# Optimization experiments

Measured on AMD Instinct MI355X. Metric: run time of the kernel, lower is better.

## Reference

```python
import jax, jax.numpy as jnp
import numpy as np

N_NODES = 50000
N_EDGES = 600000
N_RELS = 16
N_GRAPHS = 128
IN_DIM = 128
REL_LAYERS = [128, 256, 128]
HIDDEN = [128, 256, 128]
N_CLASSES = 8


def setup_inputs() -> dict:
    key = jax.random.key(0)
    ks = jax.random.split(key, 24)
    inp = {}
    inp["h"] = jax.random.normal(ks[0], (N_NODES, IN_DIM), dtype=jnp.float32)
    inp["src"] = jax.random.randint(ks[1], (N_EDGES,), 0, N_NODES)
    inp["dst"] = jax.random.randint(ks[2], (N_EDGES,), 0, N_NODES)
    inp["rel_types"] = jax.random.randint(ks[3], (N_EDGES,), 0, N_RELS)
    inp["graph_ids"] = jnp.sort(jax.random.randint(ks[4], (N_NODES,), 0, N_GRAPHS))
    # RelGraphConv params per layer: W_rel [R,din,dout], W_loop [din,dout], b [dout]
    prev = IN_DIM
    ki = 5
    for i, d in enumerate(REL_LAYERS):
        inp[f"W_rel{i}"] = jax.random.normal(ks[ki], (N_RELS, prev, d), dtype=jnp.float32) * 0.05
        inp[f"W_loop{i}"] = jax.random.normal(ks[ki + 1], (prev, d), dtype=jnp.float32) * 0.05
        inp[f"b{i}"] = jnp.zeros((d,), dtype=jnp.float32)
        prev = d
        ki += 2
    for i, d in enumerate(HIDDEN):
        inp[f"Wh{i}"] = jax.random.normal(ks[ki], (prev, d), dtype=jnp.float32) * 0.05
        inp[f"bh{i}"] = jnp.zeros((d,), dtype=jnp.float32)
        prev = d
        ki += 1
    inp["Wc"] = jax.random.normal(ks[ki], (prev, N_CLASSES), dtype=jnp.float32) * 0.05
    inp["bc"] = jnp.zeros((N_CLASSES,), dtype=jnp.float32)
    return inp


def _rel_graph_conv(h, src, dst, rel, W_rel, W_loop, b):
    # transform every node under every relation: [R, N, dout]
    t = jnp.einsum("nd,rde->rne", h, W_rel)
    msgs = t[rel, src]  # [E, dout] gather per edge
    agg = jax.ops.segment_sum(msgs, dst, num_segments=h.shape[0])
    return jax.nn.relu(agg + h @ W_loop + b)  # self-loop + bias (DGL defaults)


def _forward(h, src, dst, rel_types, graph_ids,
             W_rel0, W_loop0, b0, W_rel1, W_loop1, b1, W_rel2, W_loop2, b2,
             Wh0, bh0, Wh1, bh1, Wh2, bh2, Wc, bc):
    h = h.astype(jnp.float32)
    for Wr, Wl, b in ((W_rel0, W_loop0, b0), (W_rel1, W_loop1, b1), (W_rel2, W_loop2, b2)):
        h = _rel_graph_conv(h, src, dst, rel_types, Wr, Wl, b)
    # dgl.mean_nodes: per-graph mean pooling
    sums = jax.ops.segment_sum(h, graph_ids, num_segments=N_GRAPHS)
    cnts = jax.ops.segment_sum(jnp.ones((h.shape[0],), h.dtype), graph_ids, num_segments=N_GRAPHS)
    hg = sums / jnp.maximum(cnts, 1.0)[:, None]
    for W, b in ((Wh0, bh0), (Wh1, bh1), (Wh2, bh2)):
        hg = jax.nn.relu(hg @ W + b)
    return jax.nn.softmax(hg @ Wc + bc, axis=1)


def reference(h, src, dst, rel_types, graph_ids,
              W_rel0, W_loop0, b0, W_rel1, W_loop1, b1, W_rel2, W_loop2, b2,
              Wh0, bh0, Wh1, bh1, Wh2, bh2, Wc, bc):
    return _forward(h, src, dst, rel_types, graph_ids,
                    W_rel0, W_loop0, b0, W_rel1, W_loop1, b1, W_rel2, W_loop2, b2,
                    Wh0, bh0, Wh1, bh1, Wh2, bh2, Wc, bc)
```

## Files before the change

### kernel.cpp

```cpp
#include <hip/hip_runtime.h>
#include <stdint.h>

#define NN 50000
#define NE 600000
#define NR 16
#define NG 128
#define TS 128
#define SCAN_B 512
#define NB_SCAN ((NN + SCAN_B - 1) / SCAN_B)
#define MAXB 1024

typedef short bf16x8 __attribute__((ext_vector_type(8)));
typedef float f32x4 __attribute__((ext_vector_type(4)));

static __device__ __forceinline__ unsigned short f2bf(float x) {
    unsigned int b = __float_as_uint(x);
    b += 0x7FFFu + ((b >> 16) & 1u);
    return (unsigned short)(b >> 16);
}
static __device__ __forceinline__ float bf2f(unsigned short u) {
    return __uint_as_float(((unsigned int)u) << 16);
}


__global__ void k_hist(const int* __restrict__ rel, const int* __restrict__ dst,
                       int* __restrict__ bcnt, int* __restrict__ ncnt, int npc, int B) {
    __shared__ int lh[MAXB];
    for (int i = threadIdx.x; i < B; i += 256) lh[i] = 0;
    __syncthreads();
    for (int e = blockIdx.x * blockDim.x + threadIdx.x; e < NE; e += gridDim.x * blockDim.x) {
        int d = dst[e];
        atomicAdd(&lh[(d / npc) * NR + rel[e]], 1);
        atomicAdd(&ncnt[d], 1);
    }
    __syncthreads();
    for (int i = threadIdx.x; i < B; i += 256) atomicAdd(&bcnt[i], lh[i]);
}

__global__ void k_scan1(const int* __restrict__ ncnt, int* __restrict__ bsum) {
    __shared__ int s[SCAN_B];
    int i = blockIdx.x * SCAN_B + threadIdx.x;
    s[threadIdx.x] = (i < NN) ? ncnt[i] : 0;
    __syncthreads();
    for (int off = SCAN_B / 2; off > 0; off >>= 1) {
        if (threadIdx.x < off) s[threadIdx.x] += s[threadIdx.x + off];
        __syncthreads();
    }
    if (threadIdx.x == 0) bsum[blockIdx.x] = s[0];
}

__global__ void k_scan2(const int* __restrict__ bsum, int* __restrict__ bpref, int* __restrict__ rowptr) {
    if (threadIdx.x == 0 && blockIdx.x == 0) {
        int run = 0;
        for (int b = 0; b < NB_SCAN; ++b) { bpref[b] = run; run += bsum[b]; }
        rowptr[NN] = run;
    }
}

__global__ void k_scan3(const int* __restrict__ ncnt, const int* __restrict__ bpref,
                        int* __restrict__ rowptr) {
    __shared__ int s[SCAN_B];
    int i = blockIdx.x * SCAN_B + threadIdx.x;
    int val = (i < NN) ? ncnt[i] : 0;
    s[threadIdx.x] = val;
    __syncthreads();
    for (int off = 1; off < SCAN_B; off <<= 1) {
        int x = (threadIdx.x >= off) ? s[threadIdx.x - off] : 0;
        __syncthreads();
        s[threadIdx.x] += x;
        __syncthreads();
    }
    if (i < NN) rowptr[i] = bpref[blockIdx.x] + s[threadIdx.x] - val;
}

__global__ __launch_bounds__(1024)
void k_scan_buckets(const int* __restrict__ bcnt, int B, int npc,
                    const int* __restrict__ rowptr,
                    int* __restrict__ boff, int* __restrict__ tstart,
                    int4* __restrict__ tilemap) {
    __shared__ int s1[MAXB], s2[MAXB];
    __shared__ int e_ex[MAXB + 1], t_ex[MAXB + 1];
    int tid = threadIdx.x;
    int v1 = (tid < B) ? bcnt[tid] : 0;
    int v2 = (v1 + TS - 1) / TS;
    s1[tid] = v1; s2[tid] = v2;
    __syncthreads();
    for (int off = 1; off < MAXB; off <<= 1) {
        int a1 = (tid >= off) ? s1[tid - off] : 0;
        int a2 = (tid >= off) ? s2[tid - off] : 0;
        __syncthreads();
        s1[tid] += a1; s2[tid] += a2;
        __syncthreads();
    }
    if (tid < B) {
        e_ex[tid] = s1[tid] - v1;
        t_ex[tid] = s2[tid] - v2;
        boff[tid] = e_ex[tid];
        tstart[tid] = t_ex[tid];
        if (tid == B - 1) {
            e_ex[B] = s1[tid]; t_ex[B] = s2[tid];
            boff[B] = s1[tid]; tstart[B] = s2[tid];
        }
    }
    __syncthreads();
    int T = t_ex[B];
    for (int t = tid; t < T; t += 1024) {
        int lo = 0, hi = B - 1;
        while (lo < hi) {
            int mid = (lo + hi + 1) >> 1;
            if (t_ex[mid] <= t) lo = mid; else hi = mid - 1;
        }
        int b = lo;
        int tt = t - t_ex[b];
        int v1b = e_ex[b + 1] - e_ex[b];
        int rem = v1b - tt * TS;
        int cnt = rem < TS ? rem : TS;
        int chunk = b >> 4;
        int nstart = chunk * npc; if (nstart > NN) nstart = NN;
        tilemap[t] = make_int4(b & (NR - 1), e_ex[b] + tt * TS, cnt, rowptr[nstart]);
    }
}

__global__ void k_scatter(const int* __restrict__ rel, const int* __restrict__ dst,
                          const int* __restrict__ src,
                          const int* __restrict__ boff, int* __restrict__ cursor,
                          const int* __restrict__ rowptr, int* __restrict__ ncur,
                          int* __restrict__ srcs, int* __restrict__ dpos, int npc, int B) {
    __shared__ int lh[MAXB];
    const int CH = 4096;
    int e0 = blockIdx.x * CH;
    for (int i = threadIdx.x; i < B; i += 256) lh[i] = 0;
    __syncthreads();
    for (int i = threadIdx.x; i < CH; i += 256) {
        int e = e0 + i;
        if (e < NE) atomicAdd(&lh[(dst[e] / npc) * NR + rel[e]], 1);
    }
    __syncthreads();
    for (int i = threadIdx.x; i < B; i += 256) {
        int c = lh[i];
        lh[i] = (c > 0) ? atomicAdd(&cursor[i], c) : 0;
    }
    __syncthreads();
    for (int i = threadIdx.x; i < CH; i += 256) {
        int e = e0 + i;
        if (e < NE) {
            int d = dst[e];
            int b = (d / npc) * NR + rel[e];
            int p = boff[b] + atomicAdd(&lh[b], 1);
            int pd = rowptr[d] + atomicAdd(&ncur[d], 1);
            srcs[p] = src[e];
            dpos[p] = pd;
        }
    }
}


__global__ void k_hconv(const float* __restrict__ h, unsigned short* __restrict__ hb, int n4) {
    int i = blockIdx.x * 256 + threadIdx.x;
    if (i < n4) {
        float4 v = reinterpret_cast<const float4*>(h)[i];
        ushort4 o = { f2bf(v.x), f2bf(v.y), f2bf(v.z), f2bf(v.w) };
        reinterpret_cast<ushort4*>(hb)[i] = o;
    }
}

__global__ void k_wconv_all(const float* Wr0, const float* Wr1, const float* Wr2,
                            const float* Wl0, const float* Wl1, const float* Wl2,
                            unsigned short* Wt0, unsigned short* Wt1, unsigned short* Wt2,
                            unsigned short* Wlt0, unsigned short* Wlt1, unsigned short* Wlt2) {
    const float* W; unsigned short* O; int R, Kd, Nd;
    switch (blockIdx.y) {
        case 0:  W = Wr0; O = Wt0;  R = NR; Kd = 128; Nd = 128; break;
        case 1:  W = Wr1; O = Wt1;  R = NR; Kd = 128; Nd = 256; break;
        case 2:  W = Wr2; O = Wt2;  R = NR; Kd = 256; Nd = 128; break;
        case 3:  W = Wl0; O = Wlt0; R = 1;  Kd = 128; Nd = 128; break;
        case 4:  W = Wl1; O = Wlt1; R = 1;  Kd = 128; Nd = 256; break;
        default: W = Wl2; O = Wlt2; R = 1;  Kd = 256; Nd = 128; break;
    }
    int total = R * Kd * Nd;
    for (int i = blockIdx.x * 256 + threadIdx.x; i < total; i += gridDim.x * 256) {
        int r = i / (Kd * Nd);
        int rem = i - r * Kd * Nd;
        int k = rem / Nd;
        int n = rem - k * Nd;
        O[((size_t)r * Nd + n) * Kd + k] = f2bf(W[i]);
    }
}


template<int K>
__global__ __launch_bounds__(256, 4)
void k_dense_mfma(const unsigned short* __restrict__ hb,
                  const unsigned short* __restrict__ Wlt,
                  const float* __restrict__ bias,
                  float* __restrict__ outbuf, int ldn) {
    __shared__ __align__(16) unsigned short As[128][72];
    __shared__ __align__(16) unsigned short Bs[128][72];
    const int tid = threadIdx.x;
    const int row0 = blockIdx.x * 128;
    const int colbase = blockIdx.y * 128;
    const int lane = tid & 63, w = tid >> 6;
    const int quad = lane >> 4, col = lane & 15;
    const int srow = tid >> 3, sk = (tid & 7) * 8;

    f32x4 acc[8][2];
#pragma unroll
    for (int i = 0; i < 8; ++i) { acc[i][0] = 0.f; acc[i][1] = 0.f; }

    for (int k0 = 0; k0 < K; k0 += 64) {
        __syncthreads();
#pragma unroll
        for (int pp = 0; pp < 4; ++pp) {
            int rw = pp * 32 + srow;
            int ar = row0 + rw; if (ar >= NN) ar = NN - 1;
            *reinterpret_cast<uint4*>(&As[rw][sk]) =
                *reinterpret_cast<const uint4*>(hb + (size_t)ar * K + k0 + sk);
            *reinterpret_cast<uint4*>(&Bs[rw][sk]) =
                *reinterpret_cast<const uint4*>(Wlt + (size_t)(colbase + rw) * K + k0 + sk);
        }
        __syncthreads();
#pragma unroll
        for (int s = 0; s < 2; ++s) {
            bf16x8 bf0 = *reinterpret_cast<const bf16x8*>(&Bs[w * 32 + col][s * 32 + quad * 8]);
            bf16x8 bf1 = *reinterpret_cast<const bf16x8*>(&Bs[w * 32 + 16 + col][s * 32 + quad * 8]);
#pragma unroll
            for (int rt = 0; rt < 8; ++rt) {
                bf16x8 af = *reinterpret_cast<const bf16x8*>(&As[rt * 16 + col][s * 32 + quad * 8]);
                acc[rt][0] = __builtin_amdgcn_mfma_f32_16x16x32_bf16(af, bf0, acc[rt][0], 0, 0, 0);
                acc[rt][1] = __builtin_amdgcn_mfma_f32_16x16x32_bf16(af, bf1, acc[rt][1], 0, 0, 0);
            }
        }
    }
    float bv0 = bias[colbase + w * 32 + col];
    float bv1 = bias[colbase + w * 32 + 16 + col];
#pragma unroll
    for (int rt = 0; rt < 8; ++rt) {
#pragma unroll
        for (int reg = 0; reg < 4; ++reg) {
            int r = row0 + rt * 16 + quad * 4 + reg;
            if (r < NN) {
                float* dp = outbuf + (size_t)r * ldn + colbase + w * 32;
                dp[col] = acc[rt][0][reg] + bv0;
                dp[16 + col] = acc[rt][1][reg] + bv1;
            }
        }
    }
}


template<int K>
__global__ __launch_bounds__(256, 4)
void k_edge_mfma(const unsigned short* __restrict__ hb,
                 const unsigned short* __restrict__ Wt,
                 int ldn, int colbase,
                 const int* __restrict__ srcs, const int* __restrict__ dpos,
                 const int4* __restrict__ tilemap, const int* __restrict__ tstart,
                 int chunkBase,
                 unsigned short* __restrict__ msg, int capRows) {
    const int tb0 = tstart[chunkBase];
    const int tend = tstart[chunkBase + NR];
    const int t = tb0 + blockIdx.x;
    if (t >= tend) return;
    const int4 tm = tilemap[t];
    const int r = tm.x, e0 = tm.y, cnt = tm.z, cES = tm.w;

    __shared__ __align__(16) unsigned short As[2][128][72];
    __shared__ int s_src[TS], s_out[TS];
    const int tid = threadIdx.x;
    if (tid < TS) {
        int ei = e0 + (tid < cnt ? tid : cnt - 1);
        s_src[tid] = srcs[ei];
        int row = dpos[ei] - cES;
        s_out[tid] = (tid < cnt && row < capRows) ? row : -1;
    }
    __syncthreads();

    const unsigned short* Wb = Wt + ((size_t)r * ldn + colbase) * K;
    const int lane = tid & 63, w = tid >> 6;
    const int quad = lane >> 4, col = lane & 15;
    const int srow = tid >> 3, sk = (tid & 7) * 8;

    int myrow[4];
#pragma unroll
    for (int q = 0; q < 4; ++q) myrow[q] = s_src[q * 32 + srow];

    f32x4 acc[8][2];
#pragma unroll
    for (int i = 0; i < 8; ++i) { acc[i][0] = 0.f; acc[i][1] = 0.f; }

    const int NCH = K / 64;
    {
        uint4 v[4];
#pragma unroll
        for (int q = 0; q < 4; ++q)
            v[q] = *reinterpret_cast<const uint4*>(hb + (size_t)myrow[q] * K + sk);
#pragma unroll
        for (int q = 0; q < 4; ++q)
            *reinterpret_cast<uint4*>(&As[0][q * 32 + srow][sk]) = v[q];
    }
    __syncthreads();
#pragma unroll
    for (int c = 0; c < NCH; ++c) {
        uint4 v[4];
        if (c + 1 < NCH) {
#pragma unroll
            for (int q = 0; q < 4; ++q)
                v[q] = *reinterpret_cast<const uint4*>(hb + (size_t)myrow[q] * K + (c + 1) * 64 + sk);
        }
#pragma unroll
        for (int k32 = 0; k32 < 2; ++k32) {
            bf16x8 bf0 = *reinterpret_cast<const bf16x8*>(
                Wb + (size_t)(w * 32 + col) * K + c * 64 + k32 * 32 + quad * 8);
            bf16x8 bf1 = *reinterpret_cast<const bf16x8*>(
                Wb + (size_t)(w * 32 + 16 + col) * K + c * 64 + k32 * 32 + quad * 8);
#pragma unroll
            for (int rt = 0; rt < 8; ++rt) {
                bf16x8 af = *reinterpret_cast<const bf16x8*>(&As[c & 1][rt * 16 + col][k32 * 32 + quad * 8]);
                acc[rt][0] = __builtin_amdgcn_mfma_f32_16x16x32_bf16(af, bf0, acc[rt][0], 0, 0, 0);
                acc[rt][1] = __builtin_amdgcn_mfma_f32_16x16x32_bf16(af, bf1, acc[rt][1], 0, 0, 0);
            }
        }
        if (c + 1 < NCH) {
#pragma unroll
            for (int q = 0; q < 4; ++q)
                *reinterpret_cast<uint4*>(&As[(c + 1) & 1][q * 32 + srow][sk]) = v[q];
        }
        __syncthreads();
    }
#pragma unroll
    for (int rt = 0; rt < 8; ++rt) {
#pragma unroll
        for (int reg = 0; reg < 4; ++reg) {
            int m = rt * 16 + quad * 4 + reg;
            int o = s_out[m];
            if (o >= 0) {
                unsigned short* dp = msg + (size_t)o * 128 + w * 32;
                dp[col] = f2bf(acc[rt][0][reg]);
                dp[16 + col] = f2bf(acc[rt][1][reg]);
            }
        }
    }
}

__global__ __launch_bounds__(256)
void k_reduce(const unsigned short* __restrict__ msg,
              const float* __restrict__ selfb, int ld_self, int co_self,
              unsigned short* __restrict__ out_bf, int ld_bf, int co_bf,
              float* __restrict__ out_f32, int ld_f32, int co_f32,
              const int* __restrict__ rowptr, int n0, int npc, int capRows) {
    int idx = blockIdx.x * 4 + (threadIdx.x >> 6);
    int n = n0 + idx;
    if (idx >= npc || n >= NN) return;
    int lane = threadIdx.x & 63;
    int cES = rowptr[n0];
    float2 acc = *reinterpret_cast<const float2*>(selfb + (size_t)n * ld_self + co_self + lane * 2);
    int j0 = rowptr[n], j1 = rowptr[n + 1];
    for (int j = j0; j < j1; ++j) {
        int rr = j - cES;
        if (rr >= capRows) break;
        unsigned int m = *reinterpret_cast<const unsigned int*>(msg + (size_t)rr * 128 + lane * 2);
        acc.x += bf2f((unsigned short)(m & 0xffffu));
        acc.y += bf2f((unsigned short)(m >> 16));
    }
    acc.x = acc.x > 0.f ? acc.x : 0.f;
    acc.y = acc.y > 0.f ? acc.y : 0.f;
    if (out_bf) {
        unsigned int o = (unsigned int)f2bf(acc.x) | ((unsigned int)f2bf(acc.y) << 16);
        *reinterpret_cast<unsigned int*>(out_bf + (size_t)n * ld_bf + co_bf + lane * 2) = o;
    }
    if (out_f32) {
        *reinterpret_cast<float2*>(out_f32 + (size_t)n * ld_f32 + co_f32 + lane * 2) = acc;
    }
}


__global__ void k_pool(const float* __restrict__ h, const int* __restrict__ gid,
                       float* __restrict__ hg, float* __restrict__ gcnt) {
    const int c = threadIdx.x;
    int n0 = blockIdx.x * 64;
    if (n0 >= NN) return;
    int end = n0 + 64; if (end > NN) end = NN;
    int cur = gid[n0];
    float run = 0.f, crun = 0.f;
    for (int n = n0; n < end; ++n) {
        int g = gid[n];
        if (g != cur) {
            atomicAdd(&hg[cur * 128 + c], run);
            if (c == 0) atomicAdd(&gcnt[cur], crun);
            run = 0.f; crun = 0.f; cur = g;
        }
        run += h[(size_t)n * 128 + c];
        crun += 1.f;
    }
    atomicAdd(&hg[cur * 128 + c], run);
    if (c == 0) atomicAdd(&gcnt[cur], crun);
}

__global__ __launch_bounds__(256)
void k_head(const float* __restrict__ hg, const float* __restrict__ gcnt,
            const float* __restrict__ Wh0, const float* __restrict__ bh0,
            const float* __restrict__ Wh1, const float* __restrict__ bh1,
            const float* __restrict__ Wh2, const float* __restrict__ bh2,
            const float* __restrict__ Wc, const float* __restrict__ bc,
            float* __restrict__ out) {
    __shared__ float x0[128], x1[128], x2[256], x3[128], sl[8];
    int g = blockIdx.x, t = threadIdx.x;
    if (t < 128) {
        float c = gcnt[g];
        x0[t] = hg[g * 128 + t] / (c > 1.f ? c : 1.f);
    }
    __syncthreads();
    if (t < 128) {
        float a = bh0[t];
        for (int k = 0; k < 128; ++k) a += x0[k] * Wh0[k * 128 + t];
        x1[t] = a > 0.f ? a : 0.f;
    }
    __syncthreads();
    {
        float a = bh1[t];
        for (int k = 0; k < 128; ++k) a += x1[k] * Wh1[k * 256 + t];
        x2[t] = a > 0.f ? a : 0.f;
    }
    __syncthreads();
    if (t < 128) {
        float a = bh2[t];
        for (int k = 0; k < 256; ++k) a += x2[k] * Wh2[k * 128 + t];
        x3[t] = a > 0.f ? a : 0.f;
    }
    __syncthreads();
    if (t < 8) {
        float a = bc[t];
        for (int k = 0; k < 128; ++k) a += x3[k] * Wc[k * 8 + t];
        sl[t] = a;
    }
    __syncthreads();
    if (t == 0) {
        float m = sl[0];
        for (int c = 1; c < 8; ++c) m = sl[c] > m ? sl[c] : m;
        float s = 0.f, e[8];
        for (int c = 0; c < 8; ++c) { e[c] = expf(sl[c] - m); s += e[c]; }
        for (int c = 0; c < 8; ++c) out[g * 8 + c] = e[c] / s;
    }
}


extern "C" void kernel_launch(void* const* d_in, const int* in_sizes, int n_in,
                              void* d_out, int out_size, void* d_ws, size_t ws_size,
                              hipStream_t stream) {
    const float* h0   = (const float*)d_in[0];
    const int* src    = (const int*)d_in[1];
    const int* dst    = (const int*)d_in[2];
    const int* rel    = (const int*)d_in[3];
    const int* gid    = (const int*)d_in[4];
    const float* Wr0  = (const float*)d_in[5];
    const float* Wl0  = (const float*)d_in[6];
    const float* b0   = (const float*)d_in[7];
    const float* Wr1  = (const float*)d_in[8];
    const float* Wl1  = (const float*)d_in[9];
    const float* b1   = (const float*)d_in[10];
    const float* Wr2  = (const float*)d_in[11];
    const float* Wl2  = (const float*)d_in[12];
    const float* b2   = (const float*)d_in[13];
    const float* Wh0  = (const float*)d_in[14];
    const float* bh0  = (const float*)d_in[15];
    const float* Wh1  = (const float*)d_in[16];
    const float* bh1  = (const float*)d_in[17];
    const float* Wh2  = (const float*)d_in[18];
    const float* bh2  = (const float*)d_in[19];
    const float* Wc   = (const float*)d_in[20];
    const float* bc   = (const float*)d_in[21];
    float* out = (float*)d_out;

    char* p = (char*)d_ws;
    auto alloc = [&](size_t bytes) { char* q = p; p += (bytes + 255) & ~(size_t)255; return q; };
    float* bufS  = (float*)alloc((size_t)NN * 256 * 4);
    unsigned short* hbA = (unsigned short*)alloc((size_t)NN * 256 * 2);
    unsigned short* hbB = (unsigned short*)alloc((size_t)NN * 128 * 2);
    unsigned short* Wt0 = (unsigned short*)alloc((size_t)NR * 128 * 128 * 2);
    unsigned short* Wt1 = (unsigned short*)alloc((size_t)NR * 256 * 128 * 2);
    unsigned short* Wt2 = (unsigned short*)alloc((size_t)NR * 128 * 256 * 2);
    unsigned short* Wlt0 = (unsigned short*)alloc((size_t)128 * 128 * 2);
    unsigned short* Wlt1 = (unsigned short*)alloc((size_t)256 * 128 * 2);
    unsigned short* Wlt2 = (unsigned short*)alloc((size_t)128 * 256 * 2);
    int* srcs    = (int*)alloc((size_t)NE * 4);
    int* dpos    = (int*)alloc((size_t)NE * 4);
    int* rowptr  = (int*)alloc((size_t)(NN + 1) * 4);
    int* bsum    = (int*)alloc(NB_SCAN * 4);
    int* bpref   = (int*)alloc(NB_SCAN * 4);
    int* boff    = (int*)alloc((MAXB + 1) * 4);
    int* tstart  = (int*)alloc((MAXB + 1) * 4);
    int4* tilemap = (int4*)alloc((size_t)(NE / TS + MAXB + 64) * 16);
    char* zbase  = p;
    int* bcnt    = (int*)alloc(MAXB * 4);
    int* cursor  = (int*)alloc(MAXB * 4);
    int* ncnt    = (int*)alloc((size_t)NN * 4);
    int* ncur    = (int*)alloc((size_t)NN * 4);
    float* hg    = (float*)alloc((size_t)NG * 128 * 4);
    float* gcnt  = (float*)alloc(NG * 4);
    size_t zlen  = (size_t)(p - zbase);
    unsigned short* msg = (unsigned short*)p;

    long long avail = (long long)ws_size - (long long)(p - (char*)d_ws);
    if (avail < (1 << 20)) avail = (1 << 20);
    long long capR64 = avail / 256;
    int C = 64;
    for (int c = 1; c <= 64; ++c) {
        double need = (double)NE / c * 1.15 + 4096.0;
        if ((double)capR64 >= need) { C = c; break; }
    }
    int npc = (NN + C - 1) / C;
    int B = C * NR;
    int capRows = capR64 > 2000000000LL ? 2000000000 : (int)capR64;
    int TPC = (int)((double)NE / C * 1.15 / TS) + NR + 8;
    int RDB = (npc + 3) / 4;

    hipMemsetAsync(zbase, 0, zlen, stream);
    k_hist<<<256, 256, 0, stream>>>(rel, dst, bcnt, ncnt, npc, B);
    k_scan1<<<NB_SCAN, SCAN_B, 0, stream>>>(ncnt, bsum);
    k_scan2<<<1, 64, 0, stream>>>(bsum, bpref, rowptr);
    k_scan3<<<NB_SCAN, SCAN_B, 0, stream>>>(ncnt, bpref, rowptr);
    k_scan_buckets<<<1, MAXB, 0, stream>>>(bcnt, B, npc, rowptr, boff, tstart, tilemap);
    k_scatter<<<(NE + 4095) / 4096, 256, 0, stream>>>(rel, dst, src, boff, cursor, rowptr, ncur, srcs, dpos, npc, B);

    k_hconv<<<(NN * 128 / 4 + 255) / 256, 256, 0, stream>>>(h0, hbA, NN * 128 / 4);
    k_wconv_all<<<dim3(512, 6), 256, 0, stream>>>(Wr0, Wr1, Wr2, Wl0, Wl1, Wl2,
                                                  Wt0, Wt1, Wt2, Wlt0, Wlt1, Wlt2);

    const int RB = (NN + TS - 1) / TS;

    k_dense_mfma<128><<<dim3(RB, 1), 256, 0, stream>>>(hbA, Wlt0, b0, bufS, 128);
    for (int c = 0; c < C; ++c) {
        k_edge_mfma<128><<<TPC, 256, 0, stream>>>(hbA, Wt0, 128, 0, srcs, dpos, tilemap, tstart, c * NR, msg, capRows);
        k_reduce<<<RDB, 256, 0, stream>>>(msg, bufS, 128, 0, hbB, 128, 0, (float*)nullptr, 0, 0, rowptr, c * npc, npc, capRows);
    }

    k_dense_mfma<128><<<dim3(RB, 2), 256, 0, stream>>>(hbB, Wlt1, b1, bufS, 256);
    for (int half = 0; half < 2; ++half) {
        for (int c = 0; c < C; ++c) {
            k_edge_mfma<128><<<TPC, 256, 0, stream>>>(hbB, Wt1, 256, half * 128, srcs, dpos, tilemap, tstart, c * NR, msg, capRows);
            k_reduce<<<RDB, 256, 0, stream>>>(msg, bufS, 256, half * 128, hbA, 256, half * 128, (float*)nullptr, 0, 0, rowptr, c * npc, npc, capRows);
        }
    }

    k_dense_mfma<256><<<dim3(RB, 1), 256, 0, stream>>>(hbA, Wlt2, b2, bufS, 128);
    for (int c = 0; c < C; ++c) {
        k_edge_mfma<256><<<TPC, 256, 0, stream>>>(hbA, Wt2, 128, 0, srcs, dpos, tilemap, tstart, c * NR, msg, capRows);
        k_reduce<<<RDB, 256, 0, stream>>>(msg, bufS, 128, 0, (unsigned short*)nullptr, 0, 0, bufS, 128, 0, rowptr, c * npc, npc, capRows);
    }

    k_pool<<<(NN + 63) / 64, 128, 0, stream>>>(bufS, gid, hg, gcnt);
    k_head<<<NG, 256, 0, stream>>>(hg, gcnt, Wh0, bh0, Wh1, bh1, Wh2, bh2, Wc, bc, out);
}
```

Measured before the change: 815.7 us.

## Process two edge tiles per block, single-buffer LDS, unroll reduce loop

The edge kernel now handles two tilemap tiles per block with a single LDS buffer and half the grid. The old double-buffered prefetch of the next K-chunk is replaced by a load-sync-compute sequence. The reduce kernel clamps the row bound once and unrolls the message accumulation by four so more loads are in flight. Fewer blocks and less LDS may help occupancy and launch cost, but dropping the prefetch exposes gather latency and halves block-level parallelism.

```diff
diff --git a/kernel.cpp b/kernel.cpp
--- a/kernel.cpp
+++ b/kernel.cpp
@@ -259,84 +259,75 @@
                  unsigned short* __restrict__ msg, int capRows) {
     const int tb0 = tstart[chunkBase];
     const int tend = tstart[chunkBase + NR];
-    const int t = tb0 + blockIdx.x;
-    if (t >= tend) return;
-    const int4 tm = tilemap[t];
-    const int r = tm.x, e0 = tm.y, cnt = tm.z, cES = tm.w;
-
-    __shared__ __align__(16) unsigned short As[2][128][72];
-    __shared__ int s_src[TS], s_out[TS];
+    const int t0 = tb0 + blockIdx.x * 2;
+    if (t0 >= tend) return;
+    const int nt = (t0 + 1 < tend) ? 2 : 1;
+
+    __shared__ __align__(16) unsigned short As[128][72];
+    __shared__ int4 s_tm[2];
+    __shared__ int s_src[2][TS], s_out[2][TS];
     const int tid = threadIdx.x;
-    if (tid < TS) {
-        int ei = e0 + (tid < cnt ? tid : cnt - 1);
-        s_src[tid] = srcs[ei];
-        int row = dpos[ei] - cES;
-        s_out[tid] = (tid < cnt && row < capRows) ? row : -1;
-    }
-    __syncthreads();
-
-    const unsigned short* Wb = Wt + ((size_t)r * ldn + colbase) * K;
+    {
+        int ti = tid >> 7;
+        int li = tid & 127;
+        if (ti < nt) {
+            int4 tm = tilemap[t0 + ti];
+            if (li == 0) s_tm[ti] = tm;
+            int ei = tm.y + (li < tm.z ? li : tm.z - 1);
+            s_src[ti][li] = srcs[ei];
+            int row = dpos[ei] - tm.w;
+            s_out[ti][li] = (li < tm.z && row < capRows) ? row : -1;
+        }
+    }
+    __syncthreads();
+
     const int lane = tid & 63, w = tid >> 6;
     const int quad = lane >> 4, col = lane & 15;
     const int srow = tid >> 3, sk = (tid & 7) * 8;
 
-    int myrow[4];
-#pragma unroll
-    for (int q = 0; q < 4; ++q) myrow[q] = s_src[q * 32 + srow];
-
-    f32x4 acc[8][2];
-#pragma unroll
-    for (int i = 0; i < 8; ++i) { acc[i][0] = 0.f; acc[i][1] = 0.f; }
-
-    const int NCH = K / 64;
-    {
-        uint4 v[4];
-#pragma unroll
-        for (int q = 0; q < 4; ++q)
-            v[q] = *reinterpret_cast<const uint4*>(hb + (size_t)myrow[q] * K + sk);
-#pragma unroll
-        for (int q = 0; q < 4; ++q)
-            *reinterpret_cast<uint4*>(&As[0][q * 32 + srow][sk]) = v[q];
-    }
-    __syncthreads();
-#pragma unroll
-    for (int c = 0; c < NCH; ++c) {
-        uint4 v[4];
-        if (c + 1 < NCH) {
+    for (int ti = 0; ti < nt; ++ti) {
+        const int r = s_tm[ti].x;
+        const unsigned short* Wb = Wt + ((size_t)r * ldn + colbase) * K;
+        int myrow[4];
+#pragma unroll
+        for (int q = 0; q < 4; ++q) myrow[q] = s_src[ti][q * 32 + srow];
+
+        f32x4 acc[8][2];
+#pragma unroll
+        for (int i = 0; i < 8; ++i) { acc[i][0] = 0.f; acc[i][1] = 0.f; }
+
+        for (int k0 = 0; k0 < K; k0 += 64) {
+            if (k0 + ti) __syncthreads();
 #pragma unroll
             for (int q = 0; q < 4; ++q)
-                v[q] = *reinterpret_cast<const uint4*>(hb + (size_t)myrow[q] * K + (c + 1) * 64 + sk);
-        }
-#pragma unroll
-        for (int k32 = 0; k32 < 2; ++k32) {
-            bf16x8 bf0 = *reinterpret_cast<const bf16x8*>(
-                Wb + (size_t)(w * 32 + col) * K + c * 64 + k32 * 32 + quad * 8);
-            bf16x8 bf1 = *reinterpret_cast<const bf16x8*>(
-                Wb + (size_t)(w * 32 + 16 + col) * K + c * 64 + k32 * 32 + quad * 8);
-#pragma unroll
-            for (int rt = 0; rt < 8; ++rt) {
-                bf16x8 af = *reinterpret_cast<const bf16x8*>(&As[c & 1][rt * 16 + col][k32 * 32 + quad * 8]);
-                acc[rt][0] = __builtin_amdgcn_mfma_f32_16x16x32_bf16(af, bf0, acc[rt][0], 0, 0, 0);
-                acc[rt][1] = __builtin_amdgcn_mfma_f32_16x16x32_bf16(af, bf1, acc[rt][1], 0, 0, 0);
+                *reinterpret_cast<uint4*>(&As[q * 32 + srow][sk]) =
+                    *reinterpret_cast<const uint4*>(hb + (size_t)myrow[q] * K + k0 + sk);
+            __syncthreads();
+#pragma unroll
+            for (int k32 = 0; k32 < 2; ++k32) {
+                bf16x8 bf0 = *reinterpret_cast<const bf16x8*>(
+                    Wb + (size_t)(w * 32 + col) * K + k0 + k32 * 32 + quad * 8);
+                bf16x8 bf1 = *reinterpret_cast<const bf16x8*>(
+                    Wb + (size_t)(w * 32 + 16 + col) * K + k0 + k32 * 32 + quad * 8);
+#pragma unroll
+                for (int rt = 0; rt < 8; ++rt) {
+                    bf16x8 af = *reinterpret_cast<const bf16x8*>(&As[rt * 16 + col][k32 * 32 + quad * 8]);
+                    acc[rt][0] = __builtin_amdgcn_mfma_f32_16x16x32_bf16(af, bf0, acc[rt][0], 0, 0, 0);
+                    acc[rt][1] = __builtin_amdgcn_mfma_f32_16x16x32_bf16(af, bf1, acc[rt][1], 0, 0, 0);
+                }
             }
         }
-        if (c + 1 < NCH) {
-#pragma unroll
-            for (int q = 0; q < 4; ++q)
-                *reinterpret_cast<uint4*>(&As[(c + 1) & 1][q * 32 + srow][sk]) = v[q];
-        }
-        __syncthreads();
-    }
-#pragma unroll
-    for (int rt = 0; rt < 8; ++rt) {
-#pragma unroll
-        for (int reg = 0; reg < 4; ++reg) {
-            int m = rt * 16 + quad * 4 + reg;
-            int o = s_out[m];
-            if (o >= 0) {
-                unsigned short* dp = msg + (size_t)o * 128 + w * 32;
-                dp[col] = f2bf(acc[rt][0][reg]);
-                dp[16 + col] = f2bf(acc[rt][1][reg]);
+#pragma unroll
+        for (int rt = 0; rt < 8; ++rt) {
+#pragma unroll
+            for (int reg = 0; reg < 4; ++reg) {
+                int m = rt * 16 + quad * 4 + reg;
+                int o = s_out[ti][m];
+                if (o >= 0) {
+                    unsigned short* dp = msg + (size_t)o * 128 + w * 32;
+                    dp[col] = f2bf(acc[rt][0][reg]);
+                    dp[16 + col] = f2bf(acc[rt][1][reg]);
+                }
             }
         }
     }
@@ -355,10 +346,21 @@
     int cES = rowptr[n0];
     float2 acc = *reinterpret_cast<const float2*>(selfb + (size_t)n * ld_self + co_self + lane * 2);
     int j0 = rowptr[n], j1 = rowptr[n + 1];
-    for (int j = j0; j < j1; ++j) {
-        int rr = j - cES;
-        if (rr >= capRows) break;
-        unsigned int m = *reinterpret_cast<const unsigned int*>(msg + (size_t)rr * 128 + lane * 2);
+    int jcap = cES + capRows; if (j1 > jcap) j1 = jcap;
+    const unsigned int* mp = reinterpret_cast<const unsigned int*>(msg) + lane;
+    int j = j0;
+    for (; j + 4 <= j1; j += 4) {
+        unsigned int m0 = mp[(size_t)(j + 0 - cES) * 64];
+        unsigned int m1 = mp[(size_t)(j + 1 - cES) * 64];
+        unsigned int m2 = mp[(size_t)(j + 2 - cES) * 64];
+        unsigned int m3 = mp[(size_t)(j + 3 - cES) * 64];
+        acc.x += bf2f((unsigned short)(m0 & 0xffffu)) + bf2f((unsigned short)(m1 & 0xffffu))
+               + bf2f((unsigned short)(m2 & 0xffffu)) + bf2f((unsigned short)(m3 & 0xffffu));
+        acc.y += bf2f((unsigned short)(m0 >> 16)) + bf2f((unsigned short)(m1 >> 16))
+               + bf2f((unsigned short)(m2 >> 16)) + bf2f((unsigned short)(m3 >> 16));
+    }
+    for (; j < j1; ++j) {
+        unsigned int m = mp[(size_t)(j - cES) * 64];
         acc.x += bf2f((unsigned short)(m & 0xffffu));
         acc.y += bf2f((unsigned short)(m >> 16));
     }
@@ -512,6 +514,7 @@
     int B = C * NR;
     int capRows = capR64 > 2000000000LL ? 2000000000 : (int)capR64;
     int TPC = (int)((double)NE / C * 1.15 / TS) + NR + 8;
+    int TPC2 = (TPC + 1) / 2;
     int RDB = (npc + 3) / 4;
 
     hipMemsetAsync(zbase, 0, zlen, stream);
@@ -530,21 +533,21 @@
 
     k_dense_mfma<128><<<dim3(RB, 1), 256, 0, stream>>>(hbA, Wlt0, b0, bufS, 128);
     for (int c = 0; c < C; ++c) {
-        k_edge_mfma<128><<<TPC, 256, 0, stream>>>(hbA, Wt0, 128, 0, srcs, dpos, tilemap, tstart, c * NR, msg, capRows);
+        k_edge_mfma<128><<<TPC2, 256, 0, stream>>>(hbA, Wt0, 128, 0, srcs, dpos, tilemap, tstart, c * NR, msg, capRows);
         k_reduce<<<RDB, 256, 0, stream>>>(msg, bufS, 128, 0, hbB, 128, 0, (float*)nullptr, 0, 0, rowptr, c * npc, npc, capRows);
     }
 
     k_dense_mfma<128><<<dim3(RB, 2), 256, 0, stream>>>(hbB, Wlt1, b1, bufS, 256);
     for (int half = 0; half < 2; ++half) {
         for (int c = 0; c < C; ++c) {
-            k_edge_mfma<128><<<TPC, 256, 0, stream>>>(hbB, Wt1, 256, half * 128, srcs, dpos, tilemap, tstart, c * NR, msg, capRows);
+            k_edge_mfma<128><<<TPC2, 256, 0, stream>>>(hbB, Wt1, 256, half * 128, srcs, dpos, tilemap, tstart, c * NR, msg, capRows);
             k_reduce<<<RDB, 256, 0, stream>>>(msg, bufS, 256, half * 128, hbA, 256, half * 128, (float*)nullptr, 0, 0, rowptr, c * npc, npc, capRows);
         }
     }
 
     k_dense_mfma<256><<<dim3(RB, 1), 256, 0, stream>>>(hbA, Wlt2, b2, bufS, 128);
     for (int c = 0; c < C; ++c) {
-        k_edge_mfma<256><<<TPC, 256, 0, stream>>>(hbA, Wt2, 128, 0, srcs, dpos, tilemap, tstart, c * NR, msg, capRows);
+        k_edge_mfma<256><<<TPC2, 256, 0, stream>>>(hbA, Wt2, 128, 0, srcs, dpos, tilemap, tstart, c * NR, msg, capRows);
         k_reduce<<<RDB, 256, 0, stream>>>(msg, bufS, 128, 0, (unsigned short*)nullptr, 0, 0, bufS, 128, 0, rowptr, c * npc, npc, capRows);
     }
 
```

After: 813.3 us. Within noise of the previous version (-0.3%).
